# Optimization experiments

Measured on AMD Instinct MI355X. Metric: run time of the kernel, lower is better.

## Reference

```python
import jax, jax.numpy as jnp
import numpy as np

NUM_HEADS = 16
HEAD_DIM = 64
HIDDEN = NUM_HEADS * HEAD_DIM  # 1024
Q_DIM = 512
KV_DIM = 256


def setup_inputs() -> dict:
    key = jax.random.key(0)
    k1, k2, k3, k4, k5, k6 = jax.random.split(key, 6)
    B, I, J = 64, 128, 512  # num_assets, num_latents, window_size
    q = jax.random.normal(k1, (B, I, Q_DIM), dtype=jnp.float32)
    kv = jax.random.normal(k2, (B, J, KV_DIM), dtype=jnp.float32)
    # Linear weights stored as (in, out); fan-in scaled init
    Wq = jax.random.normal(k3, (Q_DIM, HIDDEN), dtype=jnp.float32) / np.sqrt(Q_DIM)
    Wkv = jax.random.normal(k4, (KV_DIM, 2 * HIDDEN), dtype=jnp.float32) / np.sqrt(KV_DIM)
    Wo = jax.random.normal(k5, (HIDDEN, Q_DIM), dtype=jnp.float32) / np.sqrt(HIDDEN)
    bo = jax.random.normal(k6, (Q_DIM,), dtype=jnp.float32) * 0.01
    return {"q": q, "kv": kv, "Wq": Wq, "Wkv": Wkv, "Wo": Wo, "bo": bo}


def reference(q, kv, Wq, Wkv, Wo, bo):
    B, I, _ = q.shape
    J = kv.shape[1]
    scale = HEAD_DIM ** -0.5
    query = q @ Wq                              # (B, I, HIDDEN)
    k, v = jnp.split(kv @ Wkv, 2, axis=-1)      # each (B, J, HIDDEN)
    qh = query.reshape(B, I, NUM_HEADS, HEAD_DIM).transpose(0, 2, 1, 3)  # bhid
    kh = k.reshape(B, J, NUM_HEADS, HEAD_DIM).transpose(0, 2, 1, 3)      # bhjd
    vh = v.reshape(B, J, NUM_HEADS, HEAD_DIM).transpose(0, 2, 1, 3)      # bhjd
    scores = jnp.einsum('bhid,bhjd->bhij', qh, kh) * scale
    attn = jax.nn.softmax(scores, axis=-1)
    out = jnp.einsum('bhij,bhjd->bhid', attn, vh)
    out = out.transpose(0, 2, 1, 3).reshape(B, I, HIDDEN)
    return out @ Wo + bo
```

## Files before the change

### kernel.cpp

```cpp
#include <hip/hip_runtime.h>
#include <stdint.h>

typedef unsigned short ushort_t;
typedef __attribute__((ext_vector_type(8))) short short8;
typedef __attribute__((ext_vector_type(4))) float floatx4;
typedef __attribute__((ext_vector_type(4))) float floatv4;
typedef __attribute__((ext_vector_type(4))) unsigned short ushortv4;


__device__ __forceinline__ ushort_t f2bf(float x) {
    union { float f; unsigned u; } v; v.f = x;
    unsigned r = v.u + 0x7fffu + ((v.u >> 16) & 1u);
    return (ushort_t)(r >> 16);
}

__device__ __forceinline__ void gl_lds16(const ushort_t* g, ushort_t* l) {
    __builtin_amdgcn_global_load_lds(
        (const __attribute__((address_space(1))) void*)g,
        (__attribute__((address_space(3))) void*)l, 16, 0, 0);
}

__global__ __launch_bounds__(256) void prep_kernel(
    const float* __restrict__ q, const float* __restrict__ kv,
    const float* __restrict__ Wq, const float* __restrict__ Wkv,
    const float* __restrict__ Wo,
    ushort_t* __restrict__ qA, ushort_t* __restrict__ kvA,
    ushort_t* __restrict__ WqT, ushort_t* __restrict__ WkvT,
    ushort_t* __restrict__ WoT)
{
    __shared__ ushort_t tileS[64 * 68];
    const int bid = blockIdx.x;
    const int tid = threadIdx.x;
    if (bid < 4096) {
        int t = bid * 256 + tid;
        floatv4 v = ((const floatv4*)q)[t];
        ushortv4 o;
        o[0] = f2bf(v[0]); o[1] = f2bf(v[1]); o[2] = f2bf(v[2]); o[3] = f2bf(v[3]);
        ((ushortv4*)qA)[t] = o;
        return;
    }
    if (bid < 12288) {
        int t = (bid - 4096) * 256 + tid;
        floatv4 v = ((const floatv4*)kv)[t];
        ushortv4 o;
        o[0] = f2bf(v[0]); o[1] = f2bf(v[1]); o[2] = f2bf(v[2]); o[3] = f2bf(v[3]);
        ((ushortv4*)kvA)[t] = o;
        return;
    }
    const float* src; ushort_t* dst; int K, N, kt, nt; float scale = 1.0f;
    if (bid < 12416)      { int tl = bid - 12288; src = Wq;  dst = WqT;  K = 512;  N = 1024; kt = tl >> 4; nt = tl & 15; scale = 0.125f; }
    else if (bid < 12544) { int tl = bid - 12416; src = Wkv; dst = WkvT; K = 256;  N = 2048; kt = tl >> 5; nt = tl & 31; }
    else                  { int tl = bid - 12544; src = Wo;  dst = WoT;  K = 1024; N = 512;  kt = tl >> 3; nt = tl & 7;  }
#pragma unroll
    for (int t = 0; t < 4; t++) {
        int e = t * 256 + tid;
        int row = e >> 4, c4 = e & 15;
        floatv4 v = *(const floatv4*)&src[(size_t)(kt * 64 + row) * N + nt * 64 + c4 * 4];
        ushortv4 o;
        o[0] = f2bf(v[0] * scale); o[1] = f2bf(v[1] * scale);
        o[2] = f2bf(v[2] * scale); o[3] = f2bf(v[3] * scale);
        *(ushortv4*)&tileS[row * 68 + c4 * 4] = o;
    }
    __syncthreads();
#pragma unroll
    for (int t = 0; t < 4; t++) {
        int e = t * 256 + tid;
        int orow = e >> 4, c4 = e & 15;
        ushortv4 o;
#pragma unroll
        for (int e2 = 0; e2 < 4; e2++) o[e2] = tileS[(c4 * 4 + e2) * 68 + orow];
        *(ushortv4*)&dst[(size_t)(nt * 64 + orow) * K + kt * 64 + c4 * 4] = o;
    }
}

__global__ __launch_bounds__(256, 3) void gemm_bt_kernel(
    const ushort_t* __restrict__ A, const ushort_t* __restrict__ Bt,
    int M, int N, int K, int gx, int gy, int emode,
    ushort_t* __restrict__ out_a,
    float* __restrict__ out_f, const float* __restrict__ bias)
{
    __shared__ ushort_t smem[16896];
    ushort_t* sA = smem;
    ushort_t* sB = smem + 8192;
    ushort_t* sT = smem;

    const int bid  = blockIdx.x;
    const int xcd  = bid & 7;
    const int slot = bid >> 3;
    const int band = gy >> 3;
    const int by   = xcd * band + slot % band;
    const int bx   = slot / band;

    const int tid  = threadIdx.x;
    const int lane = tid & 63;
    const int w    = tid >> 6;
    const int quad = lane >> 4;
    const int l15  = lane & 15;
    const int wr   = w >> 1, wc = w & 1;
    const int m0 = by * 128;
    const int n0 = bx * 128;

    const int rsub = lane >> 3;
    const int c8   = lane & 7;
    const int wrow = w * 32;

    floatx4 acc[4][4];
#pragma unroll
    for (int i = 0; i < 4; i++)
#pragma unroll
        for (int j = 0; j < 4; j++) acc[i][j] = (floatx4){0.f, 0.f, 0.f, 0.f};

    for (int k0 = 0; k0 < K; k0 += 64) {
        __syncthreads();
#pragma unroll
        for (int t = 0; t < 4; t++) {
            int rg = wrow + t * 8;
            gl_lds16(&A[(size_t)(m0 + rg + rsub) * K + k0 + c8 * 8], &sA[rg * 64]);
            gl_lds16(&Bt[(size_t)(n0 + rg + rsub) * K + k0 + c8 * 8], &sB[rg * 64]);
        }
        __syncthreads();
#pragma unroll
        for (int ks = 0; ks < 64; ks += 32) {
            short8 af[4], bf[4];
#pragma unroll
            for (int i = 0; i < 4; i++)
                af[i] = *(const short8*)&sA[(wr * 64 + i * 16 + l15) * 64 + ks + quad * 8];
#pragma unroll
            for (int j = 0; j < 4; j++)
                bf[j] = *(const short8*)&sB[(wc * 64 + j * 16 + l15) * 64 + ks + quad * 8];
#pragma unroll
            for (int i = 0; i < 4; i++)
#pragma unroll
                for (int j = 0; j < 4; j++)
                    acc[i][j] = __builtin_amdgcn_mfma_f32_16x16x32_bf16(
                        af[i], bf[j], acc[i][j], 0, 0, 0);
        }
    }

    if (emode == 2) {
#pragma unroll
        for (int i = 0; i < 4; i++)
#pragma unroll
            for (int j = 0; j < 4; j++)
#pragma unroll
                for (int r = 0; r < 4; r++) {
                    int grow = m0 + wr * 64 + i * 16 + quad * 4 + r;
                    int gcol = n0 + wc * 64 + j * 16 + l15;
                    out_f[(size_t)grow * N + gcol] = acc[i][j][r] + bias[gcol];
                }
        return;
    }

    __syncthreads();
#pragma unroll
    for (int i = 0; i < 4; i++)
#pragma unroll
        for (int j = 0; j < 4; j++)
#pragma unroll
            for (int r = 0; r < 4; r++) {
                int row = wr * 64 + i * 16 + quad * 4 + r;
                int col = wc * 64 + j * 16 + l15;
                sT[row * 132 + col] = f2bf(acc[i][j][r]);
            }
    __syncthreads();
#pragma unroll
    for (int it = 0; it < 8; it++) {
        int idx = it * 256 + tid;
        int row = idx >> 4, chunk = idx & 15;
        short8 v = *(const short8*)&sT[row * 132 + chunk * 8];
        *(short8*)&out_a[(size_t)(m0 + row) * 1024 + n0 + chunk * 8] = v;
    }
}

__global__ __launch_bounds__(512, 4) void fattn_kernel(
    const ushort_t* __restrict__ QA,
    const ushort_t* __restrict__ WQ,
    const ushort_t* __restrict__ KV,
    const ushort_t* __restrict__ W,
    ushort_t* __restrict__ O)
{
    __shared__ ushort_t smem[35328];
    ushort_t* sKV = smem;
    ushort_t* sKc = smem + 16896;
    ushort_t* sVt = smem + 21504;
    ushort_t* sP  = smem + 26112;
    ushort_t* sQ  = smem;
    ushort_t* sW  = smem + 17408;

    const int bid  = blockIdx.x;
    const int xcd  = bid & 7;
    const int slot = bid >> 3;
    const int b = xcd * 8 + (slot & 7);
    const int h = slot >> 3;

    const int tid  = threadIdx.x;
    const int lane = tid & 63, w = tid >> 6;
    const int quad = lane >> 4, l15 = lane & 15;

    ushort_t* sp = &sP[w * 1152];

    const ushort_t* qb = &QA[(size_t)b * 128 * 512];
    const ushort_t* wq = &WQ[(size_t)h * 64 * 512];
    floatx4 qacc[4];
#pragma unroll
    for (int nt = 0; nt < 4; nt++) qacc[nt] = (floatx4){0.f, 0.f, 0.f, 0.f};

    for (int kc = 0; kc < 4; kc++) {
        if (kc) __syncthreads();
#pragma unroll
        for (int t = 0; t < 4; t++) {
            int c = tid + t * 512;
            int row = c >> 4, cc = c & 15;
            *(short8*)&sQ[row * 136 + cc * 8] =
                *(const short8*)&qb[(size_t)row * 512 + kc * 128 + cc * 8];
        }
#pragma unroll
        for (int t = 0; t < 2; t++) {
            int c = tid + t * 512;
            int row = c >> 4, cc = c & 15;
            *(short8*)&sW[row * 136 + cc * 8] =
                *(const short8*)&wq[(size_t)row * 512 + kc * 128 + cc * 8];
        }
        __syncthreads();
#pragma unroll
        for (int ks = 0; ks < 4; ks++) {
            short8 af = *(const short8*)&sQ[(w * 16 + l15) * 136 + ks * 32 + quad * 8];
#pragma unroll
            for (int nt = 0; nt < 4; nt++) {
                short8 bfr = *(const short8*)&sW[(nt * 16 + l15) * 136 + ks * 32 + quad * 8];
                qacc[nt] = __builtin_amdgcn_mfma_f32_16x16x32_bf16(af, bfr, qacc[nt], 0, 0, 0);
            }
        }
    }
    __syncthreads();

#pragma unroll
    for (int nt = 0; nt < 4; nt++)
#pragma unroll
        for (int r = 0; r < 4; r++)
            sp[(quad * 4 + r) * 72 + nt * 16 + l15] = f2bf(qacc[nt][r]);
    short8 aq0 = *(const short8*)&sp[l15 * 72 + quad * 8];
    short8 aq1 = *(const short8*)&sp[l15 * 72 + 32 + quad * 8];

    short8 wf[8];
    {
        int n = w * 16 + l15;
        int grow = (n < 64) ? (h * 64 + n) : (1024 + h * 64 + (n - 64));
        const ushort_t* wp = &W[(size_t)grow * 256 + quad * 8];
#pragma unroll
        for (int ks = 0; ks < 8; ks++)
            wf[ks] = *(const short8*)(wp + ks * 32);
    }

    float lsum[4];
    floatx4 acc_o[4];
#pragma unroll
    for (int r = 0; r < 4; r++) lsum[r] = 0.f;
#pragma unroll
    for (int dt = 0; dt < 4; dt++) acc_o[dt] = (floatx4){0.f, 0.f, 0.f, 0.f};

    for (int ch = 0; ch < 8; ch++) {
        const int j0 = ch * 64;
#pragma unroll
        for (int t = 0; t < 4; t++) {
            int c = tid + t * 512;
            int row = c >> 5, cc = c & 31;
            *(short8*)&sKV[row * 264 + cc * 8] =
                *(const short8*)&KV[(size_t)(b * 512 + j0 + row) * 256 + cc * 8];
        }
        __syncthreads();

        floatx4 pacc[4];
#pragma unroll
        for (int jt = 0; jt < 4; jt++) pacc[jt] = (floatx4){0.f, 0.f, 0.f, 0.f};
#pragma unroll
        for (int ks = 0; ks < 8; ks++) {
            short8 af[4];
#pragma unroll
            for (int jt = 0; jt < 4; jt++)
                af[jt] = *(const short8*)&sKV[(jt * 16 + l15) * 264 + ks * 32 + quad * 8];
#pragma unroll
            for (int jt = 0; jt < 4; jt++)
                pacc[jt] = __builtin_amdgcn_mfma_f32_16x16x32_bf16(
                    af[jt], wf[ks], pacc[jt], 0, 0, 0);
        }

        if (w < 4) {
            int d = w * 16 + l15;
#pragma unroll
            for (int jt = 0; jt < 4; jt++)
#pragma unroll
                for (int r = 0; r < 4; r++)
                    sKc[(jt * 16 + quad * 4 + r) * 72 + d] = f2bf(pacc[jt][r]);
        } else {
            int d = (w - 4) * 16 + l15;
#pragma unroll
            for (int jt = 0; jt < 4; jt++) {
                ushortv4 p;
#pragma unroll
                for (int r = 0; r < 4; r++) p[r] = f2bf(pacc[jt][r]);
                *(ushortv4*)&sVt[d * 72 + jt * 16 + quad * 4] = p;
            }
        }
        __syncthreads();

#pragma unroll
        for (int jt = 0; jt < 4; jt++) {
            const ushort_t* kp = &sKc[(jt * 16 + l15) * 72 + quad * 8];
            short8 bk0 = *(const short8*)kp;
            short8 bk1 = *(const short8*)(kp + 32);
            floatx4 a = (floatx4){0.f, 0.f, 0.f, 0.f};
            a = __builtin_amdgcn_mfma_f32_16x16x32_bf16(aq0, bk0, a, 0, 0, 0);
            a = __builtin_amdgcn_mfma_f32_16x16x32_bf16(aq1, bk1, a, 0, 0, 0);
            ushortv4 pk;
#pragma unroll
            for (int r = 0; r < 4; r++) {
                float p = __expf(a[r]);
                lsum[r] += p;
                pk[r] = f2bf(p);
            }
#pragma unroll
            for (int r = 0; r < 4; r++)
                sp[(quad * 4 + r) * 72 + jt * 16 + l15] = pk[r];
        }

#pragma unroll
        for (int kk = 0; kk < 2; kk++) {
            short8 ap = *(const short8*)&sp[l15 * 72 + kk * 32 + quad * 8];
#pragma unroll
            for (int dt = 0; dt < 4; dt++) {
                short8 bv = *(const short8*)&sVt[(dt * 16 + l15) * 72 + kk * 32 + quad * 8];
                acc_o[dt] = __builtin_amdgcn_mfma_f32_16x16x32_bf16(ap, bv, acc_o[dt], 0, 0, 0);
            }
        }
    }

#pragma unroll
    for (int r = 0; r < 4; r++) {
        float s = lsum[r];
#pragma unroll
        for (int off = 1; off < 16; off <<= 1) s += __shfl_xor(s, off);
        float inv = 1.0f / s;
        size_t rowo = (size_t)(b * 128 + w * 16 + quad * 4 + r) * 1024 + h * 64;
#pragma unroll
        for (int dt = 0; dt < 4; dt++)
            O[rowo + dt * 16 + l15] = f2bf(acc_o[dt][r] * inv);
    }
}

extern "C" void kernel_launch(void* const* d_in, const int* in_sizes, int n_in,
                              void* d_out, int out_size, void* d_ws, size_t ws_size,
                              hipStream_t stream) {
    const float* q   = (const float*)d_in[0];
    const float* kv  = (const float*)d_in[1];
    const float* Wq  = (const float*)d_in[2];
    const float* Wkv = (const float*)d_in[3];
    const float* Wo  = (const float*)d_in[4];
    const float* bo  = (const float*)d_in[5];
    float* out = (float*)d_out;

    char* ws = (char*)d_ws;
    ushort_t* qA    = (ushort_t*)(ws + 0);
    ushort_t* kvA   = (ushort_t*)(ws + 8388608);
    ushort_t* WqT   = (ushort_t*)(ws + 25165824);
    ushort_t* WkvT  = (ushort_t*)(ws + 26214400);
    ushort_t* WoT   = (ushort_t*)(ws + 27262976);
    ushort_t* attnO = (ushort_t*)(ws + 45088768);

    hipLaunchKernelGGL(prep_kernel, dim3(12672), dim3(256), 0, stream,
                       q, kv, Wq, Wkv, Wo, qA, kvA, WqT, WkvT, WoT);

    hipLaunchKernelGGL(fattn_kernel, dim3(1024), dim3(512), 0, stream,
                       qA, WqT, kvA, WkvT, attnO);

    hipLaunchKernelGGL(gemm_bt_kernel, dim3(256), dim3(256), 0, stream,
                       attnO, WoT, 8192, 512, 1024, 4, 64, 2, (ushort_t*)nullptr,
                       out, bo);
}
```

Measured before the change: 211.1 us.

## Fuse fp32-to-bf16 conversion of q and kv into attention kernel with register prefetch

Removes the separate conversion pass over q and kv in the prep kernel, so only the weights are transposed and converted there. The attention kernel now loads fp32 q and kv directly, converts them to bf16 when staging into shared memory, and prefetches the next chunk into registers while the current one is computed. This avoids writing and re-reading bf16 copies through HBM. In exchange, each of the 16 head blocks reads twice as many bytes per batch, and register pressure rises from the prefetch buffers.

Result: slower. 246.6 us (+16.8%).

```diff
diff --git a/kernel.cpp b/kernel.cpp
--- a/kernel.cpp
+++ b/kernel.cpp
@@ -14,6 +14,15 @@
     return (ushort_t)(r >> 16);
 }
 
+__device__ __forceinline__ short8 cvt8(floatx4 a, floatx4 b) {
+    short8 o;
+    o[0] = (short)f2bf(a[0]); o[1] = (short)f2bf(a[1]);
+    o[2] = (short)f2bf(a[2]); o[3] = (short)f2bf(a[3]);
+    o[4] = (short)f2bf(b[0]); o[5] = (short)f2bf(b[1]);
+    o[6] = (short)f2bf(b[2]); o[7] = (short)f2bf(b[3]);
+    return o;
+}
+
 __device__ __forceinline__ void gl_lds16(const ushort_t* g, ushort_t* l) {
     __builtin_amdgcn_global_load_lds(
         (const __attribute__((address_space(1))) void*)g,
@@ -21,36 +30,18 @@
 }
 
 __global__ __launch_bounds__(256) void prep_kernel(
-    const float* __restrict__ q, const float* __restrict__ kv,
     const float* __restrict__ Wq, const float* __restrict__ Wkv,
     const float* __restrict__ Wo,
-    ushort_t* __restrict__ qA, ushort_t* __restrict__ kvA,
     ushort_t* __restrict__ WqT, ushort_t* __restrict__ WkvT,
     ushort_t* __restrict__ WoT)
 {
     __shared__ ushort_t tileS[64 * 68];
     const int bid = blockIdx.x;
     const int tid = threadIdx.x;
-    if (bid < 4096) {
-        int t = bid * 256 + tid;
-        floatv4 v = ((const floatv4*)q)[t];
-        ushortv4 o;
-        o[0] = f2bf(v[0]); o[1] = f2bf(v[1]); o[2] = f2bf(v[2]); o[3] = f2bf(v[3]);
-        ((ushortv4*)qA)[t] = o;
-        return;
-    }
-    if (bid < 12288) {
-        int t = (bid - 4096) * 256 + tid;
-        floatv4 v = ((const floatv4*)kv)[t];
-        ushortv4 o;
-        o[0] = f2bf(v[0]); o[1] = f2bf(v[1]); o[2] = f2bf(v[2]); o[3] = f2bf(v[3]);
-        ((ushortv4*)kvA)[t] = o;
-        return;
-    }
     const float* src; ushort_t* dst; int K, N, kt, nt; float scale = 1.0f;
-    if (bid < 12416)      { int tl = bid - 12288; src = Wq;  dst = WqT;  K = 512;  N = 1024; kt = tl >> 4; nt = tl & 15; scale = 0.125f; }
-    else if (bid < 12544) { int tl = bid - 12416; src = Wkv; dst = WkvT; K = 256;  N = 2048; kt = tl >> 5; nt = tl & 31; }
-    else                  { int tl = bid - 12544; src = Wo;  dst = WoT;  K = 1024; N = 512;  kt = tl >> 3; nt = tl & 7;  }
+    if (bid < 128)      { int tl = bid;       src = Wq;  dst = WqT;  K = 512;  N = 1024; kt = tl >> 4; nt = tl & 15; scale = 0.125f; }
+    else if (bid < 256) { int tl = bid - 128; src = Wkv; dst = WkvT; K = 256;  N = 2048; kt = tl >> 5; nt = tl & 31; }
+    else                { int tl = bid - 256; src = Wo;  dst = WoT;  K = 1024; N = 512;  kt = tl >> 3; nt = tl & 7;  }
 #pragma unroll
     for (int t = 0; t < 4; t++) {
         int e = t * 256 + tid;
@@ -173,9 +164,9 @@
 }
 
 __global__ __launch_bounds__(512, 4) void fattn_kernel(
-    const ushort_t* __restrict__ QA,
+    const float* __restrict__ Qf,
     const ushort_t* __restrict__ WQ,
-    const ushort_t* __restrict__ KV,
+    const float* __restrict__ KVf,
     const ushort_t* __restrict__ W,
     ushort_t* __restrict__ O)
 {
@@ -199,29 +190,54 @@
 
     ushort_t* sp = &sP[w * 1152];
 
-    const ushort_t* qb = &QA[(size_t)b * 128 * 512];
+    const float* qb = &Qf[(size_t)b * 128 * 512];
     const ushort_t* wq = &WQ[(size_t)h * 64 * 512];
     floatx4 qacc[4];
 #pragma unroll
     for (int nt = 0; nt < 4; nt++) qacc[nt] = (floatx4){0.f, 0.f, 0.f, 0.f};
 
+    floatx4 pq[8];
+    short8  pw[2];
+#pragma unroll
+    for (int t = 0; t < 4; t++) {
+        int c = tid + t * 512, row = c >> 4, cc = c & 15;
+        const float* s = &qb[(size_t)row * 512 + cc * 8];
+        pq[2 * t]     = *(const floatx4*)s;
+        pq[2 * t + 1] = *(const floatx4*)(s + 4);
+    }
+#pragma unroll
+    for (int t = 0; t < 2; t++) {
+        int c = tid + t * 512, row = c >> 4, cc = c & 15;
+        pw[t] = *(const short8*)&wq[(size_t)row * 512 + cc * 8];
+    }
+
     for (int kc = 0; kc < 4; kc++) {
         if (kc) __syncthreads();
 #pragma unroll
         for (int t = 0; t < 4; t++) {
-            int c = tid + t * 512;
-            int row = c >> 4, cc = c & 15;
-            *(short8*)&sQ[row * 136 + cc * 8] =
-                *(const short8*)&qb[(size_t)row * 512 + kc * 128 + cc * 8];
+            int c = tid + t * 512, row = c >> 4, cc = c & 15;
+            *(short8*)&sQ[row * 136 + cc * 8] = cvt8(pq[2 * t], pq[2 * t + 1]);
         }
 #pragma unroll
         for (int t = 0; t < 2; t++) {
-            int c = tid + t * 512;
-            int row = c >> 4, cc = c & 15;
-            *(short8*)&sW[row * 136 + cc * 8] =
-                *(const short8*)&wq[(size_t)row * 512 + kc * 128 + cc * 8];
+            int c = tid + t * 512, row = c >> 4, cc = c & 15;
+            *(short8*)&sW[row * 136 + cc * 8] = pw[t];
         }
         __syncthreads();
+        if (kc < 3) {
+#pragma unroll
+            for (int t = 0; t < 4; t++) {
+                int c = tid + t * 512, row = c >> 4, cc = c & 15;
+                const float* s = &qb[(size_t)row * 512 + (kc + 1) * 128 + cc * 8];
+                pq[2 * t]     = *(const floatx4*)s;
+                pq[2 * t + 1] = *(const floatx4*)(s + 4);
+            }
+#pragma unroll
+            for (int t = 0; t < 2; t++) {
+                int c = tid + t * 512, row = c >> 4, cc = c & 15;
+                pw[t] = *(const short8*)&wq[(size_t)row * 512 + (kc + 1) * 128 + cc * 8];
+            }
+        }
 #pragma unroll
         for (int ks = 0; ks < 4; ks++) {
             short8 af = *(const short8*)&sQ[(w * 16 + l15) * 136 + ks * 32 + quad * 8];
@@ -233,6 +249,16 @@
         }
     }
     __syncthreads();
+
+    const float* kvb = &KVf[(size_t)b * 512 * 256];
+    floatx4 pkv[8];
+#pragma unroll
+    for (int t = 0; t < 4; t++) {
+        int c = tid + t * 512, row = c >> 5, cc = c & 31;
+        const float* s = &kvb[(size_t)row * 256 + cc * 8];
+        pkv[2 * t]     = *(const floatx4*)s;
+        pkv[2 * t + 1] = *(const floatx4*)(s + 4);
+    }
 
 #pragma unroll
     for (int nt = 0; nt < 4; nt++)
@@ -260,15 +286,22 @@
     for (int dt = 0; dt < 4; dt++) acc_o[dt] = (floatx4){0.f, 0.f, 0.f, 0.f};
 
     for (int ch = 0; ch < 8; ch++) {
-        const int j0 = ch * 64;
 #pragma unroll
         for (int t = 0; t < 4; t++) {
-            int c = tid + t * 512;
-            int row = c >> 5, cc = c & 31;
-            *(short8*)&sKV[row * 264 + cc * 8] =
-                *(const short8*)&KV[(size_t)(b * 512 + j0 + row) * 256 + cc * 8];
+            int c = tid + t * 512, row = c >> 5, cc = c & 31;
+            *(short8*)&sKV[row * 264 + cc * 8] = cvt8(pkv[2 * t], pkv[2 * t + 1]);
         }
         __syncthreads();
+
+        if (ch < 7) {
+#pragma unroll
+            for (int t = 0; t < 4; t++) {
+                int c = tid + t * 512, row = c >> 5, cc = c & 31;
+                const float* s = &kvb[(size_t)((ch + 1) * 64 + row) * 256 + cc * 8];
+                pkv[2 * t]     = *(const floatx4*)s;
+                pkv[2 * t + 1] = *(const floatx4*)(s + 4);
+            }
+        }
 
         floatx4 pacc[4];
 #pragma unroll
@@ -360,18 +393,16 @@
     float* out = (float*)d_out;
 
     char* ws = (char*)d_ws;
-    ushort_t* qA    = (ushort_t*)(ws + 0);
-    ushort_t* kvA   = (ushort_t*)(ws + 8388608);
     ushort_t* WqT   = (ushort_t*)(ws + 25165824);
     ushort_t* WkvT  = (ushort_t*)(ws + 26214400);
     ushort_t* WoT   = (ushort_t*)(ws + 27262976);
     ushort_t* attnO = (ushort_t*)(ws + 45088768);
 
-    hipLaunchKernelGGL(prep_kernel, dim3(12672), dim3(256), 0, stream,
-                       q, kv, Wq, Wkv, Wo, qA, kvA, WqT, WkvT, WoT);
+    hipLaunchKernelGGL(prep_kernel, dim3(384), dim3(256), 0, stream,
+                       Wq, Wkv, Wo, WqT, WkvT, WoT);
 
     hipLaunchKernelGGL(fattn_kernel, dim3(1024), dim3(512), 0, stream,
-                       qA, WqT, kvA, WkvT, attnO);
+                       q, WqT, kv, WkvT, attnO);
 
     hipLaunchKernelGGL(gemm_bt_kernel, dim3(256), dim3(256), 0, stream,
                        attnO, WoT, 8192, 512, 1024, 4, 64, 2, (ushort_t*)nullptr,
```

## Use async global-to-LDS loads with XOR swizzle and prefetch next KV chunk

Applied to the files above, without the earlier changes.

Replaces register-staged global loads of Q, Wq and KV tiles with direct global_load_lds transfers into unpadded, XOR-swizzled shared memory, which removes the padding and the VGPR round-trip. The next KV chunk is issued right after the K/V projection barrier so its load overlaps the QK^T, softmax and PV work of the current chunk. This relies on sKV not overlapping the sKc/sVt/sP regions during the prefetch. It also depends on the swizzle keeping LDS bank conflicts low without padding.

Result: no change. 208.6 us (-1.2%).

```diff
diff --git a/kernel.cpp b/kernel.cpp
--- a/kernel.cpp
+++ b/kernel.cpp
@@ -179,13 +179,13 @@
     const ushort_t* __restrict__ W,
     ushort_t* __restrict__ O)
 {
-    __shared__ ushort_t smem[35328];
+    __shared__ ushort_t smem[34816];
     ushort_t* sKV = smem;
-    ushort_t* sKc = smem + 16896;
-    ushort_t* sVt = smem + 21504;
-    ushort_t* sP  = smem + 26112;
+    ushort_t* sKc = smem + 16384;
+    ushort_t* sVt = smem + 20992;
+    ushort_t* sP  = smem + 25600;
     ushort_t* sQ  = smem;
-    ushort_t* sW  = smem + 17408;
+    ushort_t* sW  = smem + 16384;
 
     const int bid  = blockIdx.x;
     const int xcd  = bid & 7;
@@ -196,8 +196,14 @@
     const int tid  = threadIdx.x;
     const int lane = tid & 63, w = tid >> 6;
     const int quad = lane >> 4, l15 = lane & 15;
+    const int swz  = (l15 & 7) << 3;
 
     ushort_t* sp = &sP[w * 1152];
+
+    const int rq = lane >> 4;
+    const int gq = l15 * 8;
+    const int rh = lane >> 5;
+    const int gk = (lane & 31) * 8;
 
     const ushort_t* qb = &QA[(size_t)b * 128 * 512];
     const ushort_t* wq = &WQ[(size_t)h * 64 * 512];
@@ -209,30 +215,44 @@
         if (kc) __syncthreads();
 #pragma unroll
         for (int t = 0; t < 4; t++) {
-            int c = tid + t * 512;
-            int row = c >> 4, cc = c & 15;
-            *(short8*)&sQ[row * 136 + cc * 8] =
-                *(const short8*)&qb[(size_t)row * 512 + kc * 128 + cc * 8];
+            int rb = w * 16 + t * 4;
+            int srow = rb + rq;
+            int scol = kc * 128 + (gq ^ ((srow & 7) << 3));
+            gl_lds16(&qb[(size_t)srow * 512 + scol], &sQ[rb * 128]);
         }
 #pragma unroll
         for (int t = 0; t < 2; t++) {
-            int c = tid + t * 512;
-            int row = c >> 4, cc = c & 15;
-            *(short8*)&sW[row * 136 + cc * 8] =
-                *(const short8*)&wq[(size_t)row * 512 + kc * 128 + cc * 8];
+            int rb = w * 8 + t * 4;
+            int srow = rb + rq;
+            int scol = kc * 128 + (gq ^ ((srow & 7) << 3));
+            gl_lds16(&wq[(size_t)srow * 512 + scol], &sW[rb * 128]);
         }
         __syncthreads();
 #pragma unroll
         for (int ks = 0; ks < 4; ks++) {
-            short8 af = *(const short8*)&sQ[(w * 16 + l15) * 136 + ks * 32 + quad * 8];
+            short8 af = *(const short8*)&sQ[(w * 16 + l15) * 128 + ((ks * 32 + quad * 8) ^ swz)];
 #pragma unroll
             for (int nt = 0; nt < 4; nt++) {
-                short8 bfr = *(const short8*)&sW[(nt * 16 + l15) * 136 + ks * 32 + quad * 8];
+                short8 bfr = *(const short8*)&sW[(nt * 16 + l15) * 128 + ((ks * 32 + quad * 8) ^ swz)];
                 qacc[nt] = __builtin_amdgcn_mfma_f32_16x16x32_bf16(af, bfr, qacc[nt], 0, 0, 0);
             }
         }
     }
     __syncthreads();
+
+    const ushort_t* kvb = &KV[(size_t)b * 512 * 256];
+#define STAGE_KV(CH)                                                          \
+    {                                                                         \
+        _Pragma("unroll")                                                     \
+        for (int t = 0; t < 4; t++) {                                         \
+            int rloc = 8 * w + 2 * t;          \
+            int srow = rloc + rh;                                             \
+            int scol = gk ^ ((srow & 7) << 3);                                \
+            gl_lds16(&kvb[(size_t)((CH) * 64 + srow) * 256 + scol],           \
+                     &sKV[rloc * 256]);                                       \
+        }                                                                     \
+    }
+    STAGE_KV(0);
 
 #pragma unroll
     for (int nt = 0; nt < 4; nt++)
@@ -260,14 +280,6 @@
     for (int dt = 0; dt < 4; dt++) acc_o[dt] = (floatx4){0.f, 0.f, 0.f, 0.f};
 
     for (int ch = 0; ch < 8; ch++) {
-        const int j0 = ch * 64;
-#pragma unroll
-        for (int t = 0; t < 4; t++) {
-            int c = tid + t * 512;
-            int row = c >> 5, cc = c & 31;
-            *(short8*)&sKV[row * 264 + cc * 8] =
-                *(const short8*)&KV[(size_t)(b * 512 + j0 + row) * 256 + cc * 8];
-        }
         __syncthreads();
 
         floatx4 pacc[4];
@@ -278,7 +290,7 @@
             short8 af[4];
 #pragma unroll
             for (int jt = 0; jt < 4; jt++)
-                af[jt] = *(const short8*)&sKV[(jt * 16 + l15) * 264 + ks * 32 + quad * 8];
+                af[jt] = *(const short8*)&sKV[(jt * 16 + l15) * 256 + ((ks * 32 + quad * 8) ^ swz)];
 #pragma unroll
             for (int jt = 0; jt < 4; jt++)
                 pacc[jt] = __builtin_amdgcn_mfma_f32_16x16x32_bf16(
@@ -303,6 +315,8 @@
             }
         }
         __syncthreads();
+
+        if (ch < 7) STAGE_KV(ch + 1);
 
 #pragma unroll
         for (int jt = 0; jt < 4; jt++) {
@@ -346,6 +360,7 @@
         for (int dt = 0; dt < 4; dt++)
             O[rowo + dt * 16 + l15] = f2bf(acc_o[dt][r] * inv);
     }
+#undef STAGE_KV
 }
 
 extern "C" void kernel_launch(void* const* d_in, const int* in_sizes, int n_in,
```
